# Kernel optimization log

Hardware: AMD Instinct MI355X
Metric: run time of the kernel (lower is better)

Reference implementation:

```python
import jax, jax.numpy as jnp
import numpy as np

N_SRC, N_TGT, N_EDGES = 100000, 50000, 1000000
S_IN, T_IN, S_OUT, T_OUT = 128, 128, 64, 64
NEG_SLOPE = 0.2


def setup_inputs() -> dict:
    key = jax.random.key(0)
    ks = jax.random.split(key, 7)
    return {
        "x_source": jax.random.normal(ks[0], (N_SRC, S_IN), jnp.float32),
        "x_target": jax.random.normal(ks[1], (N_TGT, T_IN), jnp.float32),
        "w_s": jax.random.normal(ks[2], (S_IN, T_OUT), jnp.float32) * 0.1,
        "w_t": jax.random.normal(ks[3], (T_IN, S_OUT), jnp.float32) * 0.1,
        "att_weight": jax.random.normal(ks[4], (T_OUT + S_OUT,), jnp.float32) * 0.1,
        "nbhd_values": jnp.ones((N_EDGES,), jnp.float32),
        "rows": jax.random.randint(ks[5], (N_EDGES,), 0, N_TGT, jnp.int32),  # target idx i
        "cols": jax.random.randint(ks[6], (N_EDGES,), 0, N_SRC, jnp.int32),  # source idx j
    }


def reference(x_source, x_target, w_s, w_t, att_weight, nbhd_values, rows, cols):
    n_src, n_tgt = x_source.shape[0], x_target.shape[0]
    t_out = w_s.shape[1]  # dim of s_message
    s_out = w_t.shape[1]  # dim of t_message

    s_msg = x_source @ w_s  # [n_src, t_out]
    t_msg = x_target @ w_t  # [n_tgt, s_out]

    # e_{ij} = LeakyReLU([s_msg_j || t_msg_i] . a); a = [a_s (t_out) || a_t (s_out)]
    a_s, a_t = att_weight[:t_out], att_weight[t_out:]
    # f uses permuted attention vector: [a[s_out:] || a[:s_out]] on [t_msg_j || s_msg_i]
    b_t, b_s = att_weight[s_out:], att_weight[:s_out]

    es = s_msg @ a_s  # [n_src]
    et = t_msg @ a_t  # [n_tgt]
    ft = t_msg @ b_t  # [n_tgt]
    fs = s_msg @ b_s  # [n_src]

    # s->t attention: rows are target cells (row-normalize over target rows)
    e = jax.nn.leaky_relu(es[cols] + et[rows], NEG_SLOPE)  # [E]
    e_den = jax.ops.segment_sum(e, rows, num_segments=n_tgt)
    att_st = e / e_den[rows]

    # t->s attention: transposed indices; rows are source cells
    f = jax.nn.leaky_relu(ft[rows] + fs[cols], NEG_SLOPE)  # [E]
    f_den = jax.ops.segment_sum(f, cols, num_segments=n_src)
    att_ts = f / f_den[cols]

    # Hadamard with neighborhood values, then sparse-dense aggregation
    w_st = att_st * nbhd_values  # [E]
    w_ts = att_ts * nbhd_values  # [E]

    message_on_target = jax.ops.segment_sum(w_st[:, None] * s_msg[cols], rows, num_segments=n_tgt)  # [n_tgt, t_out]
    message_on_source = jax.ops.segment_sum(w_ts[:, None] * t_msg[rows], cols, num_segments=n_src)  # [n_src, s_out]

    # update_func is None -> identity
    return message_on_source, message_on_target
```

## Files before the change

### kernel.cpp

```cpp
#include <hip/hip_runtime.h>

#define N_SRC   100000
#define N_TGT   50000
#define N_EDGES 1000000
#define NEG     0.2
#define NXCD    8
#define TPART   (N_TGT / NXCD)
#define SPART   (N_SRC / NXCD)


#define XS 129
__global__ __launch_bounds__(256) void gemm_lds4(
    const float* __restrict__ x, const float* __restrict__ w,
    const float* __restrict__ att, int att_off, int nrows,
    float* __restrict__ msg, double* __restrict__ evec)
{
    __shared__ float xs[64 * XS];
    __shared__ double eds[4][64];
    const int tid  = threadIdx.x;
    const int lane = tid & 63;
    const int part = tid >> 6;
    const int c0   = __builtin_amdgcn_readfirstlane(part << 4);
    const int row0 = blockIdx.x * 64;
    const int row  = row0 + lane;
    const bool act = row < nrows;

    #pragma unroll
    for (int it = 0; it < 8; ++it) {
        const int fid = tid + it * 256;
        const int r = fid >> 5, q = fid & 31;
        if (row0 + r < nrows) {
            const float4 v = *(const float4*)(x + (size_t)(row0 + r) * 128 + 4 * q);
            float* d = &xs[r * XS + 4 * q];
            d[0] = v.x; d[1] = v.y; d[2] = v.z; d[3] = v.w;
        }
    }
    __syncthreads();

    float acc[16];
    #pragma unroll
    for (int c = 0; c < 16; ++c) acc[c] = 0.f;

    const int xbase = lane * XS;
    for (int kc = 0; kc < 128; kc += 16) {
        #pragma unroll
        for (int kk = 0; kk < 16; ++kk) {
            const float xk = xs[xbase + kc + kk];
            const float* wr = w + (size_t)(kc + kk) * 64 + c0;
            #pragma unroll
            for (int c = 0; c < 16; ++c)
                acc[c] = fmaf(xk, wr[c], acc[c]);
        }
    }

    double e = 0.0;
    #pragma unroll
    for (int c = 0; c < 16; ++c)
        e += (double)acc[c] * (double)att[att_off + c0 + c];
    eds[part][lane] = e;
    __syncthreads();
    if (part == 0 && act)
        evec[row] = eds[0][lane] + eds[1][lane] + eds[2][lane] + eds[3][lane];

    if (act) {
        float* mo = msg + (size_t)row * 64 + c0;
        #pragma unroll
        for (int q = 0; q < 4; ++q)
            *(float4*)(mo + 4 * q) = *(float4*)(acc + 4 * q);
    }
}

__global__ __launch_bounds__(256) void hist_rank(
    const int* __restrict__ rows, const int* __restrict__ cols,
    int* __restrict__ cnt_r, int* __restrict__ cnt_c,
    int* __restrict__ rank_r, int* __restrict__ rank_c)
{
    const int i = blockIdx.x * blockDim.x + threadIdx.x;
    if (i >= N_EDGES) return;
    rank_r[i] = atomicAdd(&cnt_r[rows[i]], 1);
    rank_c[i] = atomicAdd(&cnt_c[cols[i]], 1);
}

__global__ __launch_bounds__(1024) void scan_two(
    const int* __restrict__ cnt_r, const int* __restrict__ cnt_c,
    int* __restrict__ ptr_r, int* __restrict__ ptr_c)
{
    const int n    = blockIdx.x ? N_SRC : N_TGT;
    const int* cnt = blockIdx.x ? cnt_c : cnt_r;
    int* ptr       = blockIdx.x ? ptr_c : ptr_r;
    const int tid  = threadIdx.x;
    const int lane = tid & 63, wid = tid >> 6;

    __shared__ int wsum[16];
    __shared__ int s_carry;
    if (tid == 0) s_carry = 0;
    __syncthreads();

    for (int base = 0; base < n; base += 4096) {
        const int idx = base + tid * 4;
        int4 v = make_int4(0, 0, 0, 0);
        if (idx + 3 < n) {
            v = *(const int4*)(cnt + idx);
        } else if (idx < n) {
            v.x = cnt[idx];
            if (idx + 1 < n) v.y = cnt[idx + 1];
            if (idx + 2 < n) v.z = cnt[idx + 2];
        }
        const int s = v.x + v.y + v.z + v.w;

        int p = s;
        #pragma unroll
        for (int d = 1; d < 64; d <<= 1) {
            int t = __shfl_up(p, d);
            if (lane >= d) p += t;
        }
        if (lane == 63) wsum[wid] = p;
        __syncthreads();
        if (tid == 0) {
            int a = 0;
            #pragma unroll
            for (int i = 0; i < 16; ++i) { int t = wsum[i]; wsum[i] = a; a += t; }
        }
        __syncthreads();

        int run = s_carry + wsum[wid] + (p - s);
        if (idx     < n) ptr[idx]     = run; run += v.x;
        if (idx + 1 < n) ptr[idx + 1] = run; run += v.y;
        if (idx + 2 < n) ptr[idx + 2] = run; run += v.z;
        if (idx + 3 < n) ptr[idx + 3] = run; run += v.w;

        __syncthreads();
        if (tid == 1023) s_carry = run;
        __syncthreads();
    }
    if (tid == 0) ptr[n] = s_carry;
}

__global__ __launch_bounds__(256) void scatter_part(
    const int* __restrict__ rows, const int* __restrict__ cols,
    const float* __restrict__ nbhd,
    const int* __restrict__ ptr_r, const int* __restrict__ ptr_c,
    const int* __restrict__ rank_r, const int* __restrict__ rank_c,
    unsigned long long* __restrict__ srtT, unsigned long long* __restrict__ srtS)
{
    const int xcd  = blockIdx.x & (NXCD - 1);
    const int ibx  = blockIdx.x >> 3;
    const int step = (gridDim.x >> 3) * blockDim.x;
    const int lo_r = xcd * TPART, lo_c = xcd * SPART;

    for (int i = ibx * blockDim.x + threadIdx.x; i < N_EDGES; i += step) {
        const int r = rows[i], c = cols[i];
        const bool mr = (unsigned)(r - lo_r) < TPART;
        const bool mc = (unsigned)(c - lo_c) < SPART;
        if (!(mr | mc)) continue;
        const unsigned long long nb =
            (unsigned long long)(unsigned)__float_as_int(nbhd[i]) << 32;
        if (mr) srtT[ptr_r[r] + rank_r[i]] = nb | (unsigned)c;
        if (mc) srtS[ptr_c[c] + rank_c[i]] = nb | (unsigned)r;
    }
}

__global__ __launch_bounds__(256) void gather_both(
    const int2* __restrict__ srtT, const int* __restrict__ ptr_r,
    const float* __restrict__ s_msg, float* __restrict__ msg_tgt,
    const int2* __restrict__ srtS, const int* __restrict__ ptr_c,
    const float* __restrict__ t_msg, float* __restrict__ msg_src,
    const double* __restrict__ es_d, const double* __restrict__ et_d)
{
    const int gw   = (blockIdx.x * blockDim.x + threadIdx.x) >> 6;
    const int lane = threadIdx.x & 63;

    const int2* srt; const int* ptr; const float* min_; float* out;
    const double* other_d; double base; int row;
    if (gw < N_TGT) {
        srt = srtT; ptr = ptr_r; min_ = s_msg; out = msg_tgt;
        other_d = es_d; row = gw; base = et_d[row];
    } else {
        row = gw - N_TGT;
        if (row >= N_SRC) return;
        srt = srtS; ptr = ptr_c; min_ = t_msg; out = msg_src;
        other_d = et_d; base = es_d[row];
    }

    const int b = ptr[row], e = ptr[row + 1];
    double den = 0.0;
    double a0 = 0.0, a1 = 0.0, a2 = 0.0, a3 = 0.0;

    for (int j0 = b; j0 < e; j0 += 64) {
        const int m = e - j0;
        int oidx = 0; double v = 0.0; float wf = 0.f;
        if (lane < m) {
            const int2 pay = srt[j0 + lane];
            oidx = pay.x;
            const float nb = __int_as_float(pay.y);
            const double sv = base + other_d[oidx];
            v = (sv >= 0.0) ? sv : NEG * sv;
            wf = (float)(v * (double)nb);
        }
        den += v;

        const int cnt = m < 64 ? m : 64;
        int j = 0;
        for (; j + 3 < cnt; j += 4) {
            const int   c0_ = __shfl(oidx, j);     const float w0 = __shfl(wf, j);
            const int   c1_ = __shfl(oidx, j + 1); const float w1 = __shfl(wf, j + 1);
            const int   c2_ = __shfl(oidx, j + 2); const float w2 = __shfl(wf, j + 2);
            const int   c3_ = __shfl(oidx, j + 3); const float w3 = __shfl(wf, j + 3);
            a0 += (double)w0 * (double)min_[(size_t)c0_ * 64 + lane];
            a1 += (double)w1 * (double)min_[(size_t)c1_ * 64 + lane];
            a2 += (double)w2 * (double)min_[(size_t)c2_ * 64 + lane];
            a3 += (double)w3 * (double)min_[(size_t)c3_ * 64 + lane];
        }
        for (; j < cnt; ++j) {
            const int   c = __shfl(oidx, j);
            const float w = __shfl(wf, j);
            a0 += (double)w * (double)min_[(size_t)c * 64 + lane];
        }
    }
    #pragma unroll
    for (int s = 32; s; s >>= 1) den += __shfl_xor(den, s);
    const double inv = (den != 0.0) ? 1.0 / den : 0.0;
    const double acc = (a0 + a1) + (a2 + a3);
    out[(size_t)row * 64 + lane] = (float)(acc * inv);
}

extern "C" void kernel_launch(void* const* d_in, const int* in_sizes, int n_in,
                              void* d_out, int out_size, void* d_ws, size_t ws_size,
                              hipStream_t stream)
{
    const float* x_source = (const float*)d_in[0];
    const float* x_target = (const float*)d_in[1];
    const float* w_s      = (const float*)d_in[2];
    const float* w_t      = (const float*)d_in[3];
    const float* att      = (const float*)d_in[4];
    const float* nbhd     = (const float*)d_in[5];
    const int*   rows     = (const int*)d_in[6];
    const int*   cols     = (const int*)d_in[7];

    float* out     = (float*)d_out;
    float* msg_src = out;
    float* msg_tgt = out + (size_t)N_SRC * 64;

    char* ws = (char*)d_ws;
    float*  s_msg  = (float*) (ws + 0);
    float*  t_msg  = (float*) (ws + 25600000);
    double* es_d   = (double*)(ws + 38400000);
    double* et_d   = (double*)(ws + 39200000);
    int*    cnt_r  = (int*)   (ws + 39600000);
    int*    cnt_c  = (int*)   (ws + 39800000);
    int*    ptr_r  = (int*)   (ws + 40200000);
    int*    ptr_c  = (int*)   (ws + 40400004);
    int*    rank_r = (int*)   (ws + 40800016);
    int*    rank_c = (int*)   (ws + 44800016);
    unsigned long long* srtT = (unsigned long long*)(ws + 48800016);
    unsigned long long* srtS = (unsigned long long*)(ws + 56800016);

    hipMemsetAsync(ws + 39600000, 0, 600000, stream);

    gemm_lds4<<<(N_SRC + 63) / 64, 256, 0, stream>>>(
        x_source, w_s, att, 0, N_SRC, s_msg, es_d);
    gemm_lds4<<<(N_TGT + 63) / 64, 256, 0, stream>>>(
        x_target, w_t, att, 64, N_TGT, t_msg, et_d);

    hist_rank<<<(N_EDGES + 255) / 256, 256, 0, stream>>>(
        rows, cols, cnt_r, cnt_c, rank_r, rank_c);
    scan_two<<<2, 1024, 0, stream>>>(cnt_r, cnt_c, ptr_r, ptr_c);
    scatter_part<<<2048, 256, 0, stream>>>(
        rows, cols, nbhd, ptr_r, ptr_c, rank_r, rank_c, srtT, srtS);

    gather_both<<<(N_TGT + N_SRC + 3) / 4, 256, 0, stream>>>(
        (const int2*)srtT, ptr_r, s_msg, msg_tgt,
        (const int2*)srtS, ptr_c, t_msg, msg_src, es_d, et_d);
}
```

Before: 332.9 us.

## Fuse both GEMMs with edge histogram in one interleaved launch; prefetch gather payload

Merges the two projection GEMM launches and the atomic histogram/rank kernel into a single launch. Block slots are interleaved so that, in each group of 8 blocks, 3 do GEMM tiles and 5 do histogram atomics, letting compute-bound and atomic-bound work share the GPU at the same time. It also software-prefetches the next 64-edge payload chunk in the gather loop to hide load latency. The costs are a larger LDS footprint reserved by the histogram blocks, which may lower occupancy, and extra registers in the gather kernel.

Result: slower. 353.9 us (+6.3%).

```diff
diff --git a/kernel.cpp b/kernel.cpp
--- a/kernel.cpp
+++ b/kernel.cpp
@@ -8,20 +8,54 @@
 #define TPART   (N_TGT / NXCD)
 #define SPART   (N_SRC / NXCD)
 
+#define GBLK_S  1563
+#define GBLK_T  782
+#define GBLK    (GBLK_S + GBLK_T)
+#define HBLK    ((N_EDGES + 255) / 256)
+#define NGROUP  782
+
 
 #define XS 129
-__global__ __launch_bounds__(256) void gemm_lds4(
-    const float* __restrict__ x, const float* __restrict__ w,
-    const float* __restrict__ att, int att_off, int nrows,
-    float* __restrict__ msg, double* __restrict__ evec)
+__global__ __launch_bounds__(256) void fused_gemm_hist(
+    const float* __restrict__ x_source, const float* __restrict__ x_target,
+    const float* __restrict__ w_s, const float* __restrict__ w_t,
+    const float* __restrict__ att,
+    float* __restrict__ s_msg, float* __restrict__ t_msg,
+    double* __restrict__ es_d, double* __restrict__ et_d,
+    const int* __restrict__ rows, const int* __restrict__ cols,
+    int* __restrict__ cnt_r, int* __restrict__ cnt_c,
+    int* __restrict__ rank_r, int* __restrict__ rank_c)
 {
     __shared__ float xs[64 * XS];
     __shared__ double eds[4][64];
+    const int grp  = blockIdx.x >> 3;
+    const int slot = blockIdx.x & 7;
     const int tid  = threadIdx.x;
+
+    if (slot >= 3) {
+        const int hi = grp * 5 + (slot - 3);
+        if (hi >= HBLK) return;
+        const int i = hi * 256 + tid;
+        if (i >= N_EDGES) return;
+        rank_r[i] = atomicAdd(&cnt_r[rows[i]], 1);
+        rank_c[i] = atomicAdd(&cnt_c[cols[i]], 1);
+        return;
+    }
+
+    const int gi = grp * 3 + slot;
+    if (gi >= GBLK) return;
+
+    const float* x; const float* w; int att_off, nrows, bblk;
+    float* msg; double* evec;
+    if (gi < GBLK_S) { x = x_source; w = w_s; att_off = 0;  nrows = N_SRC;
+                       msg = s_msg;  evec = es_d; bblk = gi; }
+    else             { x = x_target; w = w_t; att_off = 64; nrows = N_TGT;
+                       msg = t_msg;  evec = et_d; bblk = gi - GBLK_S; }
+
     const int lane = tid & 63;
     const int part = tid >> 6;
     const int c0   = __builtin_amdgcn_readfirstlane(part << 4);
-    const int row0 = blockIdx.x * 64;
+    const int row0 = bblk * 64;
     const int row  = row0 + lane;
     const bool act = row < nrows;
 
@@ -68,17 +102,6 @@
         for (int q = 0; q < 4; ++q)
             *(float4*)(mo + 4 * q) = *(float4*)(acc + 4 * q);
     }
-}
-
-__global__ __launch_bounds__(256) void hist_rank(
-    const int* __restrict__ rows, const int* __restrict__ cols,
-    int* __restrict__ cnt_r, int* __restrict__ cnt_c,
-    int* __restrict__ rank_r, int* __restrict__ rank_c)
-{
-    const int i = blockIdx.x * blockDim.x + threadIdx.x;
-    if (i >= N_EDGES) return;
-    rank_r[i] = atomicAdd(&cnt_r[rows[i]], 1);
-    rank_c[i] = atomicAdd(&cnt_c[cols[i]], 1);
 }
 
 __global__ __launch_bounds__(1024) void scan_two(
@@ -186,11 +209,16 @@
     double den = 0.0;
     double a0 = 0.0, a1 = 0.0, a2 = 0.0, a3 = 0.0;
 
+    int2 pay = make_int2(0, 0);
+    if (lane < e - b) pay = srt[b + lane];
+
     for (int j0 = b; j0 < e; j0 += 64) {
         const int m = e - j0;
+        int2 nxt = make_int2(0, 0);
+        if (j0 + 64 < e && lane < m - 64) nxt = srt[j0 + 64 + lane];
+
         int oidx = 0; double v = 0.0; float wf = 0.f;
         if (lane < m) {
-            const int2 pay = srt[j0 + lane];
             oidx = pay.x;
             const float nb = __int_as_float(pay.y);
             const double sv = base + other_d[oidx];
@@ -216,6 +244,7 @@
             const float w = __shfl(wf, j);
             a0 += (double)w * (double)min_[(size_t)c * 64 + lane];
         }
+        pay = nxt;
     }
     #pragma unroll
     for (int s = 32; s; s >>= 1) den += __shfl_xor(den, s);
@@ -257,13 +286,11 @@
 
     hipMemsetAsync(ws + 39600000, 0, 600000, stream);
 
-    gemm_lds4<<<(N_SRC + 63) / 64, 256, 0, stream>>>(
-        x_source, w_s, att, 0, N_SRC, s_msg, es_d);
-    gemm_lds4<<<(N_TGT + 63) / 64, 256, 0, stream>>>(
-        x_target, w_t, att, 64, N_TGT, t_msg, et_d);
-
-    hist_rank<<<(N_EDGES + 255) / 256, 256, 0, stream>>>(
+    fused_gemm_hist<<<NGROUP * 8, 256, 0, stream>>>(
+        x_source, x_target, w_s, w_t, att,
+        s_msg, t_msg, es_d, et_d,
         rows, cols, cnt_r, cnt_c, rank_r, rank_c);
+
     scan_two<<<2, 1024, 0, stream>>>(cnt_r, cnt_c, ptr_r, ptr_c);
     scatter_part<<<2048, 256, 0, stream>>>(
         rows, cols, nbhd, ptr_r, ptr_c, rank_r, rank_c, srtT, srtS);
```
